# Performance work log

Measured on AMD Instinct MI355X. Metric: run time of the kernel, lower is better.

Reference implementation:

```python
import jax, jax.numpy as jnp
import numpy as np

B, R, E, H = 1024, 1024, 1024, 512
L_ATTR, L_OBJ, L_RELA = 16, 36, 64
EPS = 1e-8


def _lstm_cell(x, h, c, Wih, Whh, bih, bhh):
    # torch.nn.LSTMCell: gates ordered i, f, g, o
    g = x @ Wih.T + bih + h @ Whh.T + bhh
    i, f, gg, o = jnp.split(g, 4, axis=1)
    c2 = jax.nn.sigmoid(f) * c + jax.nn.sigmoid(i) * jnp.tanh(gg)
    h2 = jax.nn.sigmoid(o) * jnp.tanh(c2)
    return h2, c2


def _attend(h, feats, p_feats, mask, Wq, bq, wa, ba):
    att_h = h @ Wq.T + bq                         # [B,H]
    dot = jnp.tanh(p_feats + att_h[:, None, :])   # [B,L,H]
    scores = dot @ wa + ba                        # [B,L]
    w = jax.nn.softmax(scores, axis=1)
    w = w * mask
    w = w / (w.sum(1, keepdims=True) + EPS)
    return jnp.einsum('bl,bld->bd', w, feats)     # [B,R]


def setup_inputs() -> dict:
    key = jax.random.key(0)
    ks = iter(jax.random.split(key, 64))
    n = lambda shp, s=0.02: jax.random.normal(next(ks), shp, dtype=jnp.float32) * s
    inp = {
        'xt': n((B, E), 1.0), 'fc_feats': n((B, R), 1.0),
        'state_h': n((2, B, R), 1.0), 'state_c': n((2, B, R), 1.0),
        'attr_feats': n((B, L_ATTR, R), 1.0), 'obj_feats': n((B, L_OBJ, R), 1.0),
        'rela_feats': n((B, L_RELA, R), 1.0),
        'p_attr_feats': n((B, L_ATTR, H), 1.0), 'p_obj_feats': n((B, L_OBJ, H), 1.0),
        'p_rela_feats': n((B, L_RELA, H), 1.0),
        'attr_masks': jnp.ones((B, L_ATTR), jnp.float32),
        'att_masks': jnp.ones((B, L_OBJ), jnp.float32),
        'rela_masks': jnp.ones((B, L_RELA), jnp.float32),
        'att_Wih': n((4 * R, E + 2 * R)), 'att_Whh': n((4 * R, R)),
        'att_bih': n((4 * R,)), 'att_bhh': n((4 * R,)),
        'lang_Wih': n((4 * R, 4 * R)), 'lang_Whh': n((4 * R, R)),
        'lang_bih': n((4 * R,)), 'lang_bhh': n((4 * R,)),
    }
    for p in ('attr', 'obj', 'rela'):
        inp[p + '_Wq'] = n((H, R)); inp[p + '_bq'] = n((H,))
        inp[p + '_wa'] = n((H,));   inp[p + '_ba'] = n((1,))
    return inp


def reference(xt, fc_feats, state_h, state_c, attr_feats, obj_feats, rela_feats,
              p_attr_feats, p_obj_feats, p_rela_feats, attr_masks, att_masks,
              rela_masks, att_Wih, att_Whh, att_bih, att_bhh, lang_Wih, lang_Whh,
              lang_bih, lang_bhh, attr_Wq, attr_bq, attr_wa, attr_ba, obj_Wq,
              obj_bq, obj_wa, obj_ba, rela_Wq, rela_bq, rela_wa, rela_ba):
    prev_h = state_h[-1]
    att_in = jnp.concatenate([prev_h, fc_feats, xt], axis=1)
    h_att, c_att = _lstm_cell(att_in, state_h[0], state_c[0],
                              att_Wih, att_Whh, att_bih, att_bhh)
    a_attr = _attend(h_att, attr_feats, p_attr_feats, attr_masks,
                     attr_Wq, attr_bq, attr_wa, attr_ba)
    a_obj = _attend(h_att, obj_feats, p_obj_feats, att_masks,
                    obj_Wq, obj_bq, obj_wa, obj_ba)
    a_rela = _attend(h_att, rela_feats, p_rela_feats, rela_masks,
                     rela_Wq, rela_bq, rela_wa, rela_ba)
    lang_in = jnp.concatenate([h_att, a_attr, a_obj, a_rela], axis=1)
    h_lang, c_lang = _lstm_cell(lang_in, state_h[1], state_c[1],
                                lang_Wih, lang_Whh, lang_bih, lang_bhh)
    # dropout in eval mode -> identity
    output = h_lang
    return output, jnp.stack([h_att, h_lang]), jnp.stack([c_att, c_lang])
```

## Files before the change

### kernel.cpp

```cpp
#include <hip/hip_runtime.h>
#include <math.h>

typedef _Float16 half8  __attribute__((ext_vector_type(8)));
typedef _Float16 half4v __attribute__((ext_vector_type(4)));
typedef float    f32x4  __attribute__((ext_vector_type(4)));

__device__ __forceinline__ _Float16 f2h(float f) { return (_Float16)f; }

__device__ __forceinline__ float tanh_fast(float x) {
    float e = __expf(2.f * x);
    return 1.f - 2.f / (e + 1.f);
}

#define LDSB (128 * 40)

__device__ __forceinline__ void gemm_body(
    _Float16* __restrict__ sm,
    const float* A0, const float* A1, const float* A2p, const float* A3,
    const float* A4,
    const float* W0, const float* W1, const float* W2,
    int w0cols, int w0s, int w1s, int nsel,
    _Float16* __restrict__ Cpart, int ldc,
    int kb, int kLen, int ntile, int mtile, int zout)
{
    _Float16* smA = sm;
    _Float16* smW = sm + 2 * LDSB;
    const int tid  = threadIdx.x;
    const int lane = tid & 63;
    const int wid  = tid >> 6;
    const int wm   = wid >> 1, wn = wid & 1;
    const int m0   = mtile * 128;
    const int n0   = ntile * 128;
    const int nt   = kLen >> 5;
    const int srow = tid >> 3;
    const int scol = (tid & 7) << 2;
    const int fr   = lane & 15;
    const int kq   = lane >> 4;

    const float* wsel = nullptr;
    if (nsel) {
        int sel = n0 >> 9;
        const float* Wq = (sel == 0) ? W0 : (sel == 1) ? W1 : W2;
        wsel = Wq + (size_t)((n0 & 511) + srow) * 1024 + kb + scol;
    }

    f32x4 acc[4][4] = {};
    float4 va[4], vw[4];

    auto LOADA = [&](int lk) {
        int gk = kb + lk;
        int seg = gk >> 10;
        const float* ap = (seg == 0) ? A0 : (seg == 1) ? A1 : (seg == 2) ? A2p
                        : (seg == 3) ? A3 : A4;
        ap += (size_t)(m0 + srow) * 1024 + (gk & 1023) + scol;
        #pragma unroll
        for (int p = 0; p < 4; ++p)
            va[p] = *reinterpret_cast<const float4*>(ap + (size_t)p * 32 * 1024);
    };
    auto LOADW = [&](int lk) {
        const float* wp; int wstr;
        if (nsel) {
            wp = wsel + lk; wstr = 1024;
        } else {
            int gk = kb + lk;
            if (gk < w0cols) { wp = W0 + (size_t)(n0 + srow) * w0s + gk + scol;            wstr = w0s; }
            else             { wp = W1 + (size_t)(n0 + srow) * w1s + (gk - w0cols) + scol; wstr = w1s; }
        }
        #pragma unroll
        for (int p = 0; p < 4; ++p)
            vw[p] = *reinterpret_cast<const float4*>(wp + (size_t)p * 32 * wstr);
    };
    auto WRITEA = [&](int buf) {
        _Float16* d = smA + buf * LDSB;
        #pragma unroll
        for (int p = 0; p < 4; ++p) {
            half4v h = { f2h(va[p].x), f2h(va[p].y), f2h(va[p].z), f2h(va[p].w) };
            *reinterpret_cast<half4v*>(&d[(srow + p * 32) * 40 + scol]) = h;
        }
    };
    auto WRITEW = [&](int buf) {
        _Float16* d = smW + buf * LDSB;
        #pragma unroll
        for (int p = 0; p < 4; ++p) {
            half4v h = { f2h(vw[p].x), f2h(vw[p].y), f2h(vw[p].z), f2h(vw[p].w) };
            *reinterpret_cast<half4v*>(&d[(srow + p * 32) * 40 + scol]) = h;
        }
    };
    auto DOMFMA = [&](int buf) {
        half8 af[4], bf[4];
        _Float16* sA = smA + buf * LDSB;
        _Float16* sW = smW + buf * LDSB;
        #pragma unroll
        for (int i = 0; i < 4; ++i) {
            af[i] = *reinterpret_cast<const half8*>(&sA[(wm * 64 + i * 16 + fr) * 40 + kq * 8]);
            bf[i] = *reinterpret_cast<const half8*>(&sW[(wn * 64 + i * 16 + fr) * 40 + kq * 8]);
        }
        #pragma unroll
        for (int i = 0; i < 4; ++i)
            #pragma unroll
            for (int j = 0; j < 4; ++j)
                acc[i][j] = __builtin_amdgcn_mfma_f32_16x16x32_f16(af[i], bf[j], acc[i][j], 0, 0, 0);
    };

    LOADA(0); LOADW(0);
    WRITEA(0); WRITEW(0);
    __syncthreads();
    int cur = 0;
    for (int it = 0; it < nt - 1; ++it) {
        LOADA((it + 1) * 32);
        LOADW((it + 1) * 32);
        DOMFMA(cur);
        WRITEA(cur ^ 1);
        WRITEW(cur ^ 1);
        __syncthreads();
        cur ^= 1;
    }
    DOMFMA(cur);

    _Float16* cp = Cpart + (size_t)zout * 1024ull * (size_t)ldc;
    #pragma unroll
    for (int j = 0; j < 4; ++j) {
        int nc = n0 + wn * 64 + j * 16 + fr;
        #pragma unroll
        for (int i = 0; i < 4; ++i) {
            int rb = m0 + wm * 64 + i * 16 + kq * 4;
            #pragma unroll
            for (int r = 0; r < 4; ++r)
                cp[(size_t)(rb + r) * ldc + nc] = (_Float16)acc[i][j][r];
        }
    }
}

__global__ __launch_bounds__(256) void gemm_hf(
    const float* A0, const float* A1, const float* A2p, const float* A3,
    const float* A4,
    const float* W0, const float* W1, const float* W2,
    int w0cols, int w0s, int w1s, int nsel,
    _Float16* Cpart, int ldc, int kLen, int zbase)
{
    __shared__ _Float16 sm[4 * LDSB];
    gemm_body(sm, A0, A1, A2p, A3, A4, W0, W1, W2, w0cols, w0s, w1s, nsel,
              Cpart, ldc, blockIdx.z * kLen, kLen,
              blockIdx.x, blockIdx.y, zbase + blockIdx.z);
}

__global__ __launch_bounds__(256) void attend3(
    const float* __restrict__ attr_feats, const float* __restrict__ obj_feats,
    const float* __restrict__ rela_feats,
    const float* __restrict__ p_attr, const float* __restrict__ p_obj,
    const float* __restrict__ p_rela,
    const float* __restrict__ attr_masks, const float* __restrict__ att_masks,
    const float* __restrict__ rela_masks,
    const _Float16* __restrict__ q16,
    const float* __restrict__ attr_bq, const float* __restrict__ obj_bq,
    const float* __restrict__ rela_bq,
    const float* __restrict__ attr_wa, const float* __restrict__ obj_wa,
    const float* __restrict__ rela_wa,
    const float* __restrict__ attr_ba, const float* __restrict__ obj_ba,
    const float* __restrict__ rela_ba,
    float* __restrict__ a32)
{
    __shared__ float q[512];
    __shared__ float sc[64];
    __shared__ float wgt[64];
    const int b   = blockIdx.x;
    const int mod = blockIdx.y;
    const float* feats  = (mod == 0) ? attr_feats : (mod == 1) ? obj_feats  : rela_feats;
    const float* pfeats = (mod == 0) ? p_attr     : (mod == 1) ? p_obj      : p_rela;
    const float* mask   = (mod == 0) ? attr_masks : (mod == 1) ? att_masks  : rela_masks;
    const float* bq     = (mod == 0) ? attr_bq    : (mod == 1) ? obj_bq     : rela_bq;
    const float* wa     = (mod == 0) ? attr_wa    : (mod == 1) ? obj_wa     : rela_wa;
    const float* ba     = (mod == 0) ? attr_ba    : (mod == 1) ? obj_ba     : rela_ba;
    const int L         = (mod == 0) ? 16 : (mod == 1) ? 36 : 64;
    float* outa = a32 + (size_t)mod * 1024 * 1024;

    const int tid = threadIdx.x;
    const int lane = tid & 63, wid = tid >> 6;
    const _Float16* q0 = q16 + mod * 512;
    const _Float16* q1 = q16 + 1536ull * 1024 + mod * 512;
    for (int i = tid; i < 512; i += 256)
        q[i] = (float)q0[(size_t)b * 1536 + i] + (float)q1[(size_t)b * 1536 + i] + bq[i];
    __syncthreads();
    for (int l = wid; l < L; l += 4) {
        const float* pf = pfeats + ((size_t)b * L + l) * 512;
        float s = 0.f;
        #pragma unroll
        for (int h0 = 0; h0 < 512; h0 += 64) {
            int h = h0 + lane;
            s += tanh_fast(pf[h] + q[h]) * wa[h];
        }
        #pragma unroll
        for (int off = 32; off >= 1; off >>= 1) s += __shfl_xor(s, off);
        if (lane == 0) sc[l] = s + ba[0];
    }
    __syncthreads();
    if (tid < 64) {
        float v = (tid < L) ? sc[tid] : -1e30f;
        float m = v;
        #pragma unroll
        for (int off = 32; off >= 1; off >>= 1) m = fmaxf(m, __shfl_xor(m, off));
        float e = (tid < L) ? __expf(v - m) : 0.f;
        float sum = e;
        #pragma unroll
        for (int off = 32; off >= 1; off >>= 1) sum += __shfl_xor(sum, off);
        float w = e / sum;
        float wm = (tid < L) ? w * mask[(size_t)b * L + tid] : 0.f;
        float s2 = wm;
        #pragma unroll
        for (int off = 32; off >= 1; off >>= 1) s2 += __shfl_xor(s2, off);
        wgt[tid] = wm / (s2 + 1e-8f);
    }
    __syncthreads();
    const int d0 = tid * 4;
    float ax = 0.f, ay = 0.f, az = 0.f, aw = 0.f;
    for (int l = 0; l < L; ++l) {
        float w = wgt[l];
        const float4 v = *reinterpret_cast<const float4*>(feats + ((size_t)b * L + l) * 1024 + d0);
        ax += w * v.x; ay += w * v.y; az += w * v.z; aw += w * v.w;
    }
    float4 o; o.x = ax; o.y = ay; o.z = az; o.w = aw;
    *reinterpret_cast<float4*>(outa + (size_t)b * 1024 + d0) = o;
}

__global__ __launch_bounds__(256) void lstm4(
    const _Float16* __restrict__ g, size_t zstride, int nz,
    const float* __restrict__ bih, const float* __restrict__ bhh,
    const float* __restrict__ c_prev,
    float* __restrict__ hA, float* __restrict__ hB,
    float* __restrict__ c_out)
{
    int idx = blockIdx.x * 256 + threadIdx.x;
    int b = idx >> 10, r = idx & 1023;
    size_t base = (size_t)b * 4096;
    float gi = bih[r]        + bhh[r];
    float gf = bih[1024 + r] + bhh[1024 + r];
    float gg = bih[2048 + r] + bhh[2048 + r];
    float go = bih[3072 + r] + bhh[3072 + r];
    for (int z = 0; z < nz; ++z) {
        const _Float16* gz = g + (size_t)z * zstride + base;
        gi += (float)gz[r];
        gf += (float)gz[1024 + r];
        gg += (float)gz[2048 + r];
        go += (float)gz[3072 + r];
    }
    float si = 1.f / (1.f + __expf(-gi));
    float sf = 1.f / (1.f + __expf(-gf));
    float so = 1.f / (1.f + __expf(-go));
    float c2 = sf * c_prev[idx] + si * tanh_fast(gg);
    float h2 = so * tanh_fast(c2);
    hA[idx] = h2;
    if (hB) hB[idx] = h2;
    c_out[idx] = c2;
}

extern "C" void kernel_launch(void* const* d_in, const int* in_sizes, int n_in,
                              void* d_out, int out_size, void* d_ws, size_t ws_size,
                              hipStream_t stream)
{
    const size_t BR = 1024ull * 1024ull;
    const float* xt         = (const float*)d_in[0];
    const float* fc         = (const float*)d_in[1];
    const float* state_h    = (const float*)d_in[2];
    const float* state_c    = (const float*)d_in[3];
    const float* attr_feats = (const float*)d_in[4];
    const float* obj_feats  = (const float*)d_in[5];
    const float* rela_feats = (const float*)d_in[6];
    const float* p_attr     = (const float*)d_in[7];
    const float* p_obj      = (const float*)d_in[8];
    const float* p_rela     = (const float*)d_in[9];
    const float* attr_masks = (const float*)d_in[10];
    const float* att_masks  = (const float*)d_in[11];
    const float* rela_masks = (const float*)d_in[12];
    const float* att_Wih    = (const float*)d_in[13];
    const float* att_Whh    = (const float*)d_in[14];
    const float* att_bih    = (const float*)d_in[15];
    const float* att_bhh    = (const float*)d_in[16];
    const float* lang_Wih   = (const float*)d_in[17];
    const float* lang_Whh   = (const float*)d_in[18];
    const float* lang_bih   = (const float*)d_in[19];
    const float* lang_bhh   = (const float*)d_in[20];
    const float* attr_Wq    = (const float*)d_in[21];
    const float* attr_bq    = (const float*)d_in[22];
    const float* attr_wa    = (const float*)d_in[23];
    const float* attr_ba    = (const float*)d_in[24];
    const float* obj_Wq     = (const float*)d_in[25];
    const float* obj_bq     = (const float*)d_in[26];
    const float* obj_wa     = (const float*)d_in[27];
    const float* obj_ba     = (const float*)d_in[28];
    const float* rela_Wq    = (const float*)d_in[29];
    const float* rela_bq    = (const float*)d_in[30];
    const float* rela_wa    = (const float*)d_in[31];
    const float* rela_ba    = (const float*)d_in[32];

    float* out = (float*)d_out;
    const float* h0 = state_h;
    const float* h1 = state_h + BR;
    float* h_att = out + BR;

    const bool big = ws_size >= 52428800ull;
    const int gslots = big ? 4 : 2;
    _Float16* g16 = (_Float16*)d_ws;
    _Float16* q16 = g16 + (size_t)gslots * 4ull * BR;
    float*    a32 = (float*)(q16 + 2ull * 1536 * 1024);
    float* a_attr = a32;
    float* a_obj  = a32 + BR;
    float* a_rela = a32 + 2 * BR;

    dim3 blk(256);
    const int zsplit = big ? 4 : 2;

    gemm_hf<<<dim3(32, 8, zsplit), blk, 0, stream>>>(
        h1, fc, xt, h0, h0, att_Wih, att_Whh, att_Whh,
        3072, 3072, 1024, 0, g16, 4096, 4096 / zsplit, 0);
    lstm4<<<dim3(4096), blk, 0, stream>>>(
        g16, 4ull * BR, gslots, att_bih, att_bhh, state_c,
        h_att, nullptr, out + 3 * BR);
    gemm_hf<<<dim3(12, 8, 2), blk, 0, stream>>>(
        h_att, h_att, h_att, h_att, h_att,
        attr_Wq, obj_Wq, rela_Wq, 0, 1024, 1024, 1,
        q16, 1536, 512, 0);
    attend3<<<dim3(1024, 3), blk, 0, stream>>>(
        attr_feats, obj_feats, rela_feats, p_attr, p_obj, p_rela,
        attr_masks, att_masks, rela_masks, q16,
        attr_bq, obj_bq, rela_bq, attr_wa, obj_wa, rela_wa,
        attr_ba, obj_ba, rela_ba, a32);
    gemm_hf<<<dim3(32, 8, zsplit), blk, 0, stream>>>(
        h_att, a_attr, a_obj, a_rela, h1,
        lang_Wih, lang_Whh, lang_Whh, 4096, 4096, 1024, 0,
        g16, 4096, 5120 / zsplit, 0);
    lstm4<<<dim3(4096), blk, 0, stream>>>(
        g16, 4ull * BR, gslots, lang_bih, lang_bhh, state_c + BR,
        out, out + 2 * BR, out + 4 * BR);
}
```

Measured before the change: 421.0 us.

## Split attention into a per-wave score kernel and a half-row weighted-sum kernel

Replaces the fused per-(batch,module) attend kernel with two kernels. The first gives each wavefront one (batch, position) score, using vectorized float4 loads of the projected features and the query, with no shared-memory staging of q. The second splits each batch row's weighted feature sum into two halves of 128-thread blocks, reading 8 positions at a time into two accumulators, with the longest module scheduled first. Scores pass between the kernels through a scratch region of the output buffer. This adds a kernel launch and a global round-trip for the scores.

```diff
diff --git a/kernel.cpp b/kernel.cpp
--- a/kernel.cpp
+++ b/kernel.cpp
@@ -144,13 +144,10 @@
               blockIdx.x, blockIdx.y, zbase + blockIdx.z);
 }
 
-__global__ __launch_bounds__(256) void attend3(
-    const float* __restrict__ attr_feats, const float* __restrict__ obj_feats,
-    const float* __restrict__ rela_feats,
+
+__global__ __launch_bounds__(256) void att_scores(
     const float* __restrict__ p_attr, const float* __restrict__ p_obj,
     const float* __restrict__ p_rela,
-    const float* __restrict__ attr_masks, const float* __restrict__ att_masks,
-    const float* __restrict__ rela_masks,
     const _Float16* __restrict__ q16,
     const float* __restrict__ attr_bq, const float* __restrict__ obj_bq,
     const float* __restrict__ rela_bq,
@@ -158,44 +155,54 @@
     const float* __restrict__ rela_wa,
     const float* __restrict__ attr_ba, const float* __restrict__ obj_ba,
     const float* __restrict__ rela_ba,
-    float* __restrict__ a32)
-{
-    __shared__ float q[512];
-    __shared__ float sc[64];
-    __shared__ float wgt[64];
-    const int b   = blockIdx.x;
-    const int mod = blockIdx.y;
-    const float* feats  = (mod == 0) ? attr_feats : (mod == 1) ? obj_feats  : rela_feats;
-    const float* pfeats = (mod == 0) ? p_attr     : (mod == 1) ? p_obj      : p_rela;
-    const float* mask   = (mod == 0) ? attr_masks : (mod == 1) ? att_masks  : rela_masks;
-    const float* bq     = (mod == 0) ? attr_bq    : (mod == 1) ? obj_bq     : rela_bq;
-    const float* wa     = (mod == 0) ? attr_wa    : (mod == 1) ? obj_wa     : rela_wa;
-    const float* ba     = (mod == 0) ? attr_ba    : (mod == 1) ? obj_ba     : rela_ba;
-    const int L         = (mod == 0) ? 16 : (mod == 1) ? 36 : 64;
-    float* outa = a32 + (size_t)mod * 1024 * 1024;
-
+    float* __restrict__ scg)
+{
+    const unsigned gw = blockIdx.x * 4u + (threadIdx.x >> 6);
+    const int lane = threadIdx.x & 63;
+    const unsigned b = gw / 116u;
+    const int r = (int)(gw - b * 116u);
+    const float* pf; const float* bq; const float* wa; const float* ba;
+    int l, moff, scoff, L;
+    if (r < 16)      { pf = p_attr; bq = attr_bq; wa = attr_wa; ba = attr_ba; l = r;      moff = 0;    scoff = 0;  L = 16; }
+    else if (r < 52) { pf = p_obj;  bq = obj_bq;  wa = obj_wa;  ba = obj_ba;  l = r - 16; moff = 512;  scoff = 16; L = 36; }
+    else             { pf = p_rela; bq = rela_bq; wa = rela_wa; ba = rela_ba; l = r - 52; moff = 1024; scoff = 52; L = 64; }
+
+    const float4* pf4 = reinterpret_cast<const float4*>(pf) + ((size_t)b * L + l) * 128;
+    float4 a0 = pf4[lane];
+    float4 a1 = pf4[lane + 64];
+    const _Float16* qb = q16 + (size_t)b * 1536 + moff;
+    half4v hq0a = *reinterpret_cast<const half4v*>(qb + lane * 4);
+    half4v hq0b = *reinterpret_cast<const half4v*>(qb + 256 + lane * 4);
+    const _Float16* qb1 = qb + 1536ull * 1024;
+    half4v hq1a = *reinterpret_cast<const half4v*>(qb1 + lane * 4);
+    half4v hq1b = *reinterpret_cast<const half4v*>(qb1 + 256 + lane * 4);
+    const float4* bq4 = reinterpret_cast<const float4*>(bq);
+    const float4* wa4 = reinterpret_cast<const float4*>(wa);
+    float4 b0 = bq4[lane], b1 = bq4[lane + 64];
+    float4 w0 = wa4[lane], w1 = wa4[lane + 64];
+
+    float s = tanh_fast(a0.x + (float)hq0a[0] + (float)hq1a[0] + b0.x) * w0.x
+            + tanh_fast(a0.y + (float)hq0a[1] + (float)hq1a[1] + b0.y) * w0.y
+            + tanh_fast(a0.z + (float)hq0a[2] + (float)hq1a[2] + b0.z) * w0.z
+            + tanh_fast(a0.w + (float)hq0a[3] + (float)hq1a[3] + b0.w) * w0.w
+            + tanh_fast(a1.x + (float)hq0b[0] + (float)hq1b[0] + b1.x) * w1.x
+            + tanh_fast(a1.y + (float)hq0b[1] + (float)hq1b[1] + b1.y) * w1.y
+            + tanh_fast(a1.z + (float)hq0b[2] + (float)hq1b[2] + b1.z) * w1.z
+            + tanh_fast(a1.w + (float)hq0b[3] + (float)hq1b[3] + b1.w) * w1.w;
+    #pragma unroll
+    for (int off = 32; off >= 1; off >>= 1) s += __shfl_xor(s, off);
+    if (lane == 0) scg[(size_t)b * 128 + scoff + l] = s + ba[0];
+}
+
+template<int L>
+__device__ __forceinline__ void wsum_mod(
+    const float* __restrict__ feats, const float* __restrict__ scg_b,
+    const float* __restrict__ mask_b,
+    float* __restrict__ outa, int b, int dhalf, float* wgt)
+{
     const int tid = threadIdx.x;
-    const int lane = tid & 63, wid = tid >> 6;
-    const _Float16* q0 = q16 + mod * 512;
-    const _Float16* q1 = q16 + 1536ull * 1024 + mod * 512;
-    for (int i = tid; i < 512; i += 256)
-        q[i] = (float)q0[(size_t)b * 1536 + i] + (float)q1[(size_t)b * 1536 + i] + bq[i];
-    __syncthreads();
-    for (int l = wid; l < L; l += 4) {
-        const float* pf = pfeats + ((size_t)b * L + l) * 512;
-        float s = 0.f;
-        #pragma unroll
-        for (int h0 = 0; h0 < 512; h0 += 64) {
-            int h = h0 + lane;
-            s += tanh_fast(pf[h] + q[h]) * wa[h];
-        }
-        #pragma unroll
-        for (int off = 32; off >= 1; off >>= 1) s += __shfl_xor(s, off);
-        if (lane == 0) sc[l] = s + ba[0];
-    }
-    __syncthreads();
     if (tid < 64) {
-        float v = (tid < L) ? sc[tid] : -1e30f;
+        float v = (tid < L) ? scg_b[tid] : -1e30f;
         float m = v;
         #pragma unroll
         for (int off = 32; off >= 1; off >>= 1) m = fmaxf(m, __shfl_xor(m, off));
@@ -204,22 +211,76 @@
         #pragma unroll
         for (int off = 32; off >= 1; off >>= 1) sum += __shfl_xor(sum, off);
         float w = e / sum;
-        float wm = (tid < L) ? w * mask[(size_t)b * L + tid] : 0.f;
+        float wm = (tid < L) ? w * mask_b[tid] : 0.f;
         float s2 = wm;
         #pragma unroll
         for (int off = 32; off >= 1; off >>= 1) s2 += __shfl_xor(s2, off);
         wgt[tid] = wm / (s2 + 1e-8f);
     }
     __syncthreads();
-    const int d0 = tid * 4;
-    float ax = 0.f, ay = 0.f, az = 0.f, aw = 0.f;
-    for (int l = 0; l < L; ++l) {
-        float w = wgt[l];
-        const float4 v = *reinterpret_cast<const float4*>(feats + ((size_t)b * L + l) * 1024 + d0);
-        ax += w * v.x; ay += w * v.y; az += w * v.z; aw += w * v.w;
-    }
-    float4 o; o.x = ax; o.y = ay; o.z = az; o.w = aw;
+
+    const int d0 = dhalf * 512 + tid * 4;
+    const float* fp = feats + (size_t)b * L * 1024 + d0;
+    f32x4 acc0 = {0.f, 0.f, 0.f, 0.f};
+    f32x4 acc1 = {0.f, 0.f, 0.f, 0.f};
+    constexpr int NFULL = L / 8;
+    #pragma unroll
+    for (int g = 0; g < NFULL; ++g) {
+        float4 v0 = *reinterpret_cast<const float4*>(fp + (size_t)(g * 8 + 0) * 1024);
+        float4 v1 = *reinterpret_cast<const float4*>(fp + (size_t)(g * 8 + 1) * 1024);
+        float4 v2 = *reinterpret_cast<const float4*>(fp + (size_t)(g * 8 + 2) * 1024);
+        float4 v3 = *reinterpret_cast<const float4*>(fp + (size_t)(g * 8 + 3) * 1024);
+        float4 v4 = *reinterpret_cast<const float4*>(fp + (size_t)(g * 8 + 4) * 1024);
+        float4 v5 = *reinterpret_cast<const float4*>(fp + (size_t)(g * 8 + 5) * 1024);
+        float4 v6 = *reinterpret_cast<const float4*>(fp + (size_t)(g * 8 + 6) * 1024);
+        float4 v7 = *reinterpret_cast<const float4*>(fp + (size_t)(g * 8 + 7) * 1024);
+        float w0 = wgt[g * 8 + 0], w1 = wgt[g * 8 + 1], w2 = wgt[g * 8 + 2], w3 = wgt[g * 8 + 3];
+        float w4 = wgt[g * 8 + 4], w5 = wgt[g * 8 + 5], w6 = wgt[g * 8 + 6], w7 = wgt[g * 8 + 7];
+        acc0[0] += w0 * v0.x + w2 * v2.x + w4 * v4.x + w6 * v6.x;
+        acc0[1] += w0 * v0.y + w2 * v2.y + w4 * v4.y + w6 * v6.y;
+        acc0[2] += w0 * v0.z + w2 * v2.z + w4 * v4.z + w6 * v6.z;
+        acc0[3] += w0 * v0.w + w2 * v2.w + w4 * v4.w + w6 * v6.w;
+        acc1[0] += w1 * v1.x + w3 * v3.x + w5 * v5.x + w7 * v7.x;
+        acc1[1] += w1 * v1.y + w3 * v3.y + w5 * v5.y + w7 * v7.y;
+        acc1[2] += w1 * v1.z + w3 * v3.z + w5 * v5.z + w7 * v7.z;
+        acc1[3] += w1 * v1.w + w3 * v3.w + w5 * v5.w + w7 * v7.w;
+    }
+    #pragma unroll
+    for (int lg = NFULL * 8; lg < L; lg += 2) {
+        float4 v0 = *reinterpret_cast<const float4*>(fp + (size_t)lg * 1024);
+        float4 v1 = *reinterpret_cast<const float4*>(fp + (size_t)(lg + 1) * 1024);
+        float w0 = wgt[lg], w1 = wgt[lg + 1];
+        acc0[0] += w0 * v0.x; acc0[1] += w0 * v0.y; acc0[2] += w0 * v0.z; acc0[3] += w0 * v0.w;
+        acc1[0] += w1 * v1.x; acc1[1] += w1 * v1.y; acc1[2] += w1 * v1.z; acc1[3] += w1 * v1.w;
+    }
+    float4 o;
+    o.x = acc0[0] + acc1[0]; o.y = acc0[1] + acc1[1];
+    o.z = acc0[2] + acc1[2]; o.w = acc0[3] + acc1[3];
     *reinterpret_cast<float4*>(outa + (size_t)b * 1024 + d0) = o;
+}
+
+__global__ __launch_bounds__(128) void att_wsum(
+    const float* __restrict__ attr_feats, const float* __restrict__ obj_feats,
+    const float* __restrict__ rela_feats,
+    const float* __restrict__ attr_masks, const float* __restrict__ att_masks,
+    const float* __restrict__ rela_masks,
+    const float* __restrict__ scg,
+    float* __restrict__ a32)
+{
+    __shared__ float wgt[64];
+    const int bid = blockIdx.x;
+    const int sub = bid >> 11;
+    const int b   = (bid & 2047) >> 1;
+    const int dh  = bid & 1;
+    if (sub == 0)
+        wsum_mod<64>(rela_feats, scg + (size_t)b * 128 + 52, rela_masks + (size_t)b * 64,
+                     a32 + 2ull * 1024 * 1024, b, dh, wgt);
+    else if (sub == 1)
+        wsum_mod<36>(obj_feats,  scg + (size_t)b * 128 + 16, att_masks + (size_t)b * 36,
+                     a32 + 1024ull * 1024, b, dh, wgt);
+    else
+        wsum_mod<16>(attr_feats, scg + (size_t)b * 128 + 0,  attr_masks + (size_t)b * 16,
+                     a32, b, dh, wgt);
 }
 
 __global__ __launch_bounds__(256) void lstm4(
@@ -296,6 +357,7 @@
     const float* h0 = state_h;
     const float* h1 = state_h + BR;
     float* h_att = out + BR;
+    float* scg  = out;
 
     const bool big = ws_size >= 52428800ull;
     const int gslots = big ? 4 : 2;
@@ -319,11 +381,13 @@
         h_att, h_att, h_att, h_att, h_att,
         attr_Wq, obj_Wq, rela_Wq, 0, 1024, 1024, 1,
         q16, 1536, 512, 0);
-    attend3<<<dim3(1024, 3), blk, 0, stream>>>(
-        attr_feats, obj_feats, rela_feats, p_attr, p_obj, p_rela,
-        attr_masks, att_masks, rela_masks, q16,
+    att_scores<<<dim3(29696), blk, 0, stream>>>(
+        p_attr, p_obj, p_rela, q16,
         attr_bq, obj_bq, rela_bq, attr_wa, obj_wa, rela_wa,
-        attr_ba, obj_ba, rela_ba, a32);
+        attr_ba, obj_ba, rela_ba, scg);
+    att_wsum<<<dim3(6144), dim3(128), 0, stream>>>(
+        attr_feats, obj_feats, rela_feats,
+        attr_masks, att_masks, rela_masks, scg, a32);
     gemm_hf<<<dim3(32, 8, zsplit), blk, 0, stream>>>(
         h_att, a_attr, a_obj, a_rela, h1,
         lang_Wih, lang_Whh, lang_Whh, 4096, 4096, 1024, 0,
```

New measurement: 426.1 us. About the same (+1.2%).
